# Kernel optimization log

Measured on AMD Instinct MI355X. Metric: run time of the kernel, lower is better.

Reference implementation:

```python
import jax, jax.numpy as jnp
import numpy as np

H, D = 8, 32  # gat_num_heads, structure_feature_dim // heads
N_CFG, E_CFG = 20000, 320000
N_DFG, E_DFG = 20000, 320000


def _gat(x, src, dst, lin, a_s, a_d, b):
    # PyG GATConv (concat=True), inference (dropout off). src/dst include self-loops.
    N = x.shape[0]
    xw = (x @ lin).reshape(N, H, D)              # [N,H,D]
    sc_s = (xw * a_s).sum(-1)                    # [N,H] att_src scores
    sc_d = (xw * a_d).sum(-1)                    # [N,H] att_dst scores
    alpha = jax.nn.leaky_relu(sc_s[src] + sc_d[dst], 0.2)   # [E,H]
    m = jax.lax.stop_gradient(jax.ops.segment_max(alpha, dst, num_segments=N))
    e = jnp.exp(alpha - m[dst])
    s = jax.ops.segment_sum(e, dst, num_segments=N)
    w = e / s[dst]                               # softmax over incoming edges per dst
    out = jax.ops.segment_sum(xw[src] * w[..., None], dst, num_segments=N)
    return out.reshape(N, H * D) + b


def _gat_stack(x, ei, params):
    N = x.shape[0]
    loops = jnp.arange(N)
    src = jnp.concatenate([ei[0], loops])        # add_self_loops=True (PyG default)
    dst = jnp.concatenate([ei[1], loops])
    for p in params:
        x = jax.nn.relu(_gat(x, src, dst, *p))
    return x.mean(0, keepdims=True)              # global_mean_pool -> [1, 256]


def _mha(x, in_w, in_b, out_w, out_b):
    # torch nn.MultiheadAttention, seq_len=1, batch=1, x:[1,256]
    qkv = x @ in_w.T + in_b                      # [1, 3*256]
    q, k, v = jnp.split(qkv, 3, axis=-1)
    q = q.reshape(1, H, D); k = k.reshape(1, H, D); v = v.reshape(1, H, D)
    scores = (q * k).sum(-1, keepdims=True) / jnp.sqrt(jnp.float32(D))
    attn = jax.nn.softmax(scores, axis=0)        # key length 1
    return (attn * v).reshape(1, H * D) @ out_w.T + out_b


def setup_inputs():
    key = jax.random.key(0)
    ks = iter(jax.random.split(key, 40))
    d = {}
    d['cfg_x'] = jax.random.normal(next(ks), (N_CFG, 64), jnp.float32)
    d['dfg_x'] = jax.random.normal(next(ks), (N_DFG, 32), jnp.float32)
    d['cfg_ei'] = jax.random.randint(next(ks), (2, E_CFG), 0, N_CFG)
    d['dfg_ei'] = jax.random.randint(next(ks), (2, E_DFG), 0, N_DFG)
    for name, in0 in (('cfg', 64), ('dfg', 32)):
        for i in range(3):
            fi = in0 if i == 0 else H * D
            s = 1.0 / np.sqrt(fi)
            d[f'{name}_lin{i}'] = jax.random.normal(next(ks), (fi, H * D), jnp.float32) * s
            d[f'{name}_as{i}'] = jax.random.normal(next(ks), (H, D), jnp.float32) * s
            d[f'{name}_ad{i}'] = jax.random.normal(next(ks), (H, D), jnp.float32) * s
            d[f'{name}_b{i}'] = jnp.zeros((H * D,), jnp.float32)
    E = H * D
    d['mha_in_w'] = jax.random.normal(next(ks), (3 * E, E), jnp.float32) / np.sqrt(E)
    d['mha_in_b'] = jnp.zeros((3 * E,), jnp.float32)
    d['mha_out_w'] = jax.random.normal(next(ks), (E, E), jnp.float32) / np.sqrt(E)
    d['mha_out_b'] = jnp.zeros((E,), jnp.float32)
    d['fus_w'] = jax.random.normal(next(ks), (E, 2 * E), jnp.float32) / np.sqrt(2 * E)
    d['fus_b'] = jnp.zeros((E,), jnp.float32)
    return d


def reference(cfg_x, dfg_x, cfg_ei, dfg_ei,
              cfg_lin0, cfg_as0, cfg_ad0, cfg_b0,
              cfg_lin1, cfg_as1, cfg_ad1, cfg_b1,
              cfg_lin2, cfg_as2, cfg_ad2, cfg_b2,
              dfg_lin0, dfg_as0, dfg_ad0, dfg_b0,
              dfg_lin1, dfg_as1, dfg_ad1, dfg_b1,
              dfg_lin2, dfg_as2, dfg_ad2, dfg_b2,
              mha_in_w, mha_in_b, mha_out_w, mha_out_b, fus_w, fus_b):
    cfg_p = [(cfg_lin0, cfg_as0, cfg_ad0, cfg_b0),
             (cfg_lin1, cfg_as1, cfg_ad1, cfg_b1),
             (cfg_lin2, cfg_as2, cfg_ad2, cfg_b2)]
    dfg_p = [(dfg_lin0, dfg_as0, dfg_ad0, dfg_b0),
             (dfg_lin1, dfg_as1, dfg_ad1, dfg_b1),
             (dfg_lin2, dfg_as2, dfg_ad2, dfg_b2)]
    cfg_f = _mha(_gat_stack(cfg_x, cfg_ei, cfg_p), mha_in_w, mha_in_b, mha_out_w, mha_out_b)
    dfg_f = _mha(_gat_stack(dfg_x, dfg_ei, dfg_p), mha_in_w, mha_in_b, mha_out_w, mha_out_b)
    return jnp.concatenate([cfg_f, dfg_f], axis=1) @ fus_w.T + fus_b
```

## Files before the change

### kernel.cpp

```cpp
#include <hip/hip_runtime.h>

#define NN 20000
#define ER 320000
#define ET 340000
#define CC 256
#define HH 8
#define DD 32


__global__ void zero_k(int* cnt, float* pooled) {
  int t = blockIdx.x * 256 + threadIdx.x;
  if (t < NN) cnt[t] = 0;
  if (pooled && t < 2 * CC) pooled[t] = 0.f;
}


__global__ void hist_k(const int* __restrict__ ei, int* __restrict__ cnt) {
  int e = blockIdx.x * 256 + threadIdx.x;
  if (e >= ET) return;
  int dst = (e < ER) ? ei[ER + e] : (e - ER);
  atomicAdd(&cnt[dst], 1);
}

__global__ __launch_bounds__(1024) void scan_k(const int* __restrict__ cnt,
                                               int* __restrict__ offs,
                                               int* __restrict__ cur) {
  __shared__ int part[1024];
  int t = threadIdx.x;
  const int CH = (NN + 1023) / 1024;
  int b = t * CH; if (b > NN) b = NN;
  int e = b + CH; if (e > NN) e = NN;
  int s = 0;
  for (int i = b; i < e; ++i) s += cnt[i];
  part[t] = s;
  __syncthreads();
  for (int off = 1; off < 1024; off <<= 1) {
    int v = (t >= off) ? part[t - off] : 0;
    __syncthreads();
    part[t] += v;
    __syncthreads();
  }
  int run = (t > 0) ? part[t - 1] : 0;
  for (int i = b; i < e; ++i) {
    int c = cnt[i];
    offs[i] = run;
    cur[i] = run;
    run += c;
  }
  if (t == 0) offs[NN] = ET;
}

__global__ void scatter_k(const int* __restrict__ ei, int* __restrict__ cur,
                          int* __restrict__ csr_src, int* __restrict__ csr_dst) {
  int e = blockIdx.x * 256 + threadIdx.x;
  if (e >= ET) return;
  int src, dst;
  if (e < ER) { src = ei[e]; dst = ei[ER + e]; }
  else        { src = dst = e - ER; }
  int pos = atomicAdd(&cur[dst], 1);
  csr_src[pos] = src;
  csr_dst[pos] = dst;
}

__global__ __launch_bounds__(256) void gemm_k(const float* __restrict__ X,
                                              const float* __restrict__ W,
                                              float* __restrict__ O, int K) {
  __shared__ float As[16][132];
  __shared__ float Bs[16][64];
  int tid = threadIdx.x;
  int tx = tid & 15;
  int ty = tid >> 4;
  int rb = blockIdx.y * 128, cb = blockIdx.x * 64;
  float acc[8][4] = {};

  for (int k0 = 0; k0 < K; k0 += 16) {
#pragma unroll
    for (int i = 0; i < 2; ++i) {
      int idx = tid + 256 * i;
      int row = idx >> 2;
      int kc = (idx & 3) * 4;
      int gr = rb + row; if (gr >= NN) gr = NN - 1;
      float4 v = *(const float4*)&X[(size_t)gr * K + k0 + kc];
      As[kc][row] = v.x; As[kc + 1][row] = v.y;
      As[kc + 2][row] = v.z; As[kc + 3][row] = v.w;
    }
    {
      int kk = tid >> 4, col = (tid & 15) * 4;
      float4 v = *(const float4*)&W[(size_t)(k0 + kk) * CC + cb + col];
      *(float4*)&Bs[kk][col] = v;
    }
    __syncthreads();
#pragma unroll
    for (int kk = 0; kk < 16; ++kk) {
      float4 a0 = *(const float4*)&As[kk][ty * 8];
      float4 a1 = *(const float4*)&As[kk][ty * 8 + 4];
      float4 b  = *(const float4*)&Bs[kk][tx * 4];
      float ar[8] = {a0.x, a0.y, a0.z, a0.w, a1.x, a1.y, a1.z, a1.w};
#pragma unroll
      for (int i = 0; i < 8; ++i) {
        acc[i][0] += ar[i] * b.x;
        acc[i][1] += ar[i] * b.y;
        acc[i][2] += ar[i] * b.z;
        acc[i][3] += ar[i] * b.w;
      }
    }
    __syncthreads();
  }
#pragma unroll
  for (int i = 0; i < 8; ++i) {
    int r = rb + ty * 8 + i;
    if (r < NN) {
      float4 v = make_float4(acc[i][0], acc[i][1], acc[i][2], acc[i][3]);
      *(float4*)&O[(size_t)r * CC + cb + tx * 4] = v;
    }
  }
}

__global__ void scores_k(const float* __restrict__ xw, const float* __restrict__ a_s,
                         const float* __restrict__ a_d, float* __restrict__ scs,
                         float* __restrict__ scd) {
  int t = blockIdx.x * blockDim.x + threadIdx.x;
  if (t >= NN * HH) return;
  int h = t & 7, n = t >> 3;
  const float* row = xw + (size_t)n * CC + h * DD;
  const float* as = a_s + h * DD;
  const float* ad = a_d + h * DD;
  float ss = 0.f, sd = 0.f;
#pragma unroll
  for (int d = 0; d < DD; ++d) {
    float v = row[d];
    ss += v * as[d];
    sd += v * ad[d];
  }
  scs[t] = ss;
  scd[t] = sd;
}

__global__ void alpha_k(const int* __restrict__ csr_src, const int* __restrict__ csr_dst,
                        const float* __restrict__ scs, const float* __restrict__ scd,
                        float* __restrict__ alpha) {
  int p = blockIdx.x * 256 + threadIdx.x;
  if (p >= ET) return;
  int s = csr_src[p], d = csr_dst[p];
  const float4* s4 = (const float4*)(scs + (size_t)s * 8);
  const float4* d4 = (const float4*)(scd + (size_t)d * 8);
  float4 a0 = s4[0], a1 = s4[1];
  float4 b0 = d4[0], b1 = d4[1];
  float4 r0, r1;
  float v;
  v = a0.x + b0.x; r0.x = v > 0.f ? v : 0.2f * v;
  v = a0.y + b0.y; r0.y = v > 0.f ? v : 0.2f * v;
  v = a0.z + b0.z; r0.z = v > 0.f ? v : 0.2f * v;
  v = a0.w + b0.w; r0.w = v > 0.f ? v : 0.2f * v;
  v = a1.x + b1.x; r1.x = v > 0.f ? v : 0.2f * v;
  v = a1.y + b1.y; r1.y = v > 0.f ? v : 0.2f * v;
  v = a1.z + b1.z; r1.z = v > 0.f ? v : 0.2f * v;
  v = a1.w + b1.w; r1.w = v > 0.f ? v : 0.2f * v;
  float4* o4 = (float4*)(alpha + (size_t)p * 8);
  o4[0] = r0; o4[1] = r1;
}

__global__ __launch_bounds__(256) void aggr_k(const float* __restrict__ xw,
                                              const float* __restrict__ alpha,
                                              const int* __restrict__ csr,
                                              const int* __restrict__ offs,
                                              const float* __restrict__ bias,
                                              float* __restrict__ out) {
  int n = blockIdx.x;
  int tid = threadIdx.x;
  int h = tid >> 5;
  int sl = tid & 31;
  int beg = offs[n], end = offs[n + 1];

  float m = -1e30f;
  for (int p = beg + sl; p < end; p += 32)
    m = fmaxf(m, alpha[(size_t)p * 8 + h]);
#pragma unroll
  for (int off = 16; off >= 1; off >>= 1)
    m = fmaxf(m, __shfl_xor(m, off, 64));

  float ssum = 0.f;
  for (int p = beg + sl; p < end; p += 32)
    ssum += __expf(alpha[(size_t)p * 8 + h] - m);
#pragma unroll
  for (int off = 16; off >= 1; off >>= 1)
    ssum += __shfl_xor(ssum, off, 64);
  float inv = 1.f / ssum;

  float acc = 0.f;
  int p = beg;
  for (; p + 2 <= end; p += 2) {
    int s0 = csr[p], s1 = csr[p + 1];
    float a0 = alpha[(size_t)p * 8 + h];
    float a1 = alpha[(size_t)(p + 1) * 8 + h];
    float x0 = xw[(size_t)s0 * CC + tid];
    float x1 = xw[(size_t)s1 * CC + tid];
    acc += x0 * (__expf(a0 - m) * inv);
    acc += x1 * (__expf(a1 - m) * inv);
  }
  if (p < end) {
    int s0 = csr[p];
    acc += xw[(size_t)s0 * CC + tid] * (__expf(alpha[(size_t)p * 8 + h] - m) * inv);
  }
  float r = acc + bias[tid];
  out[(size_t)n * CC + tid] = (r > 0.f) ? r : 0.f;
}

__global__ void pool_k(const float* __restrict__ x, float* __restrict__ pooled) {
  int tid = threadIdx.x;
  int rb = blockIdx.x * 250;
  float acc = 0.f;
  for (int r = 0; r < 250; ++r) acc += x[(size_t)(rb + r) * CC + tid];
  atomicAdd(&pooled[tid], acc * (1.f / NN));
}

__global__ __launch_bounds__(256) void head_k(const float* __restrict__ pooled,
                                              const float* __restrict__ in_w,
                                              const float* __restrict__ in_b,
                                              const float* __restrict__ out_w,
                                              const float* __restrict__ out_b,
                                              const float* __restrict__ fus_w,
                                              const float* __restrict__ fus_b,
                                              float* __restrict__ out) {
  __shared__ float v[2][CC];
  __shared__ float f[2][CC];
  int t = threadIdx.x;
  for (int g = 0; g < 2; ++g) {
    float a = in_b[2 * CC + t];
    const float* wr = &in_w[(size_t)(2 * CC + t) * CC];
    for (int k = 0; k < CC; ++k) a += pooled[g * CC + k] * wr[k];
    v[g][t] = a;
  }
  __syncthreads();
  for (int g = 0; g < 2; ++g) {
    float a = out_b[t];
    const float* wr = &out_w[(size_t)t * CC];
    for (int k = 0; k < CC; ++k) a += v[g][k] * wr[k];
    f[g][t] = a;
  }
  __syncthreads();
  float a = fus_b[t];
  const float* wr = &fus_w[(size_t)t * 2 * CC];
  const float* ff = &f[0][0];
  for (int k = 0; k < 2 * CC; ++k) a += ff[k] * wr[k];
  out[t] = a;
}

extern "C" void kernel_launch(void* const* d_in, const int* in_sizes, int n_in,
                              void* d_out, int out_size, void* d_ws, size_t ws_size,
                              hipStream_t stream) {
  const float* cfg_x = (const float*)d_in[0];
  const float* dfg_x = (const float*)d_in[1];
  const int* cfg_ei = (const int*)d_in[2];
  const int* dfg_ei = (const int*)d_in[3];
  const float *lin[2][3], *as_[2][3], *ad_[2][3], *bs_[2][3];
  for (int g = 0; g < 2; ++g)
    for (int i = 0; i < 3; ++i) {
      int base = 4 + g * 12 + i * 4;
      lin[g][i] = (const float*)d_in[base];
      as_[g][i] = (const float*)d_in[base + 1];
      ad_[g][i] = (const float*)d_in[base + 2];
      bs_[g][i] = (const float*)d_in[base + 3];
    }
  const float* mha_in_w = (const float*)d_in[28];
  const float* mha_in_b = (const float*)d_in[29];
  const float* mha_out_w = (const float*)d_in[30];
  const float* mha_out_b = (const float*)d_in[31];
  const float* fus_w = (const float*)d_in[32];
  const float* fus_b = (const float*)d_in[33];
  float* outp = (float*)d_out;

  char* w = (char*)d_ws;
  size_t o = 0;
  auto alloc = [&](size_t bytes) -> char* {
    char* p = w + o;
    o += (bytes + 255) & ~(size_t)255;
    return p;
  };
  float* bufA = (float*)alloc((size_t)NN * CC * 4);
  float* bufB = (float*)alloc((size_t)NN * CC * 4);
  float* scs = (float*)alloc((size_t)NN * HH * 4);
  float* scd = (float*)alloc((size_t)NN * HH * 4);
  float* alpha = (float*)alloc((size_t)ET * HH * 4);
  int* csr = (int*)alloc((size_t)ET * 4);
  int* csrd = (int*)alloc((size_t)ET * 4);
  int* offs = (int*)alloc((size_t)(NN + 1) * 4);
  int* cnt = (int*)alloc((size_t)NN * 4);
  int* cur = (int*)alloc((size_t)NN * 4);
  float* pooled = (float*)alloc(2 * CC * 4);

  const int* ei[2] = {cfg_ei, dfg_ei};
  const float* xin[2] = {cfg_x, dfg_x};
  const int K0[2] = {64, 32};

  for (int g = 0; g < 2; ++g) {
    zero_k<<<(NN + 255) / 256, 256, 0, stream>>>(cnt, g == 0 ? pooled : nullptr);
    hist_k<<<(ET + 255) / 256, 256, 0, stream>>>(ei[g], cnt);
    scan_k<<<1, 1024, 0, stream>>>(cnt, offs, cur);
    scatter_k<<<(ET + 255) / 256, 256, 0, stream>>>(ei[g], cur, csr, csrd);

    const float* x = xin[g];
    for (int l = 0; l < 3; ++l) {
      int K = (l == 0) ? K0[g] : CC;
      dim3 grid(CC / 64, (NN + 127) / 128);
      gemm_k<<<grid, 256, 0, stream>>>(x, lin[g][l], bufA, K);
      scores_k<<<(NN * HH + 255) / 256, 256, 0, stream>>>(bufA, as_[g][l], ad_[g][l],
                                                          scs, scd);
      alpha_k<<<(ET + 255) / 256, 256, 0, stream>>>(csr, csrd, scs, scd, alpha);
      aggr_k<<<NN, 256, 0, stream>>>(bufA, alpha, csr, offs, bs_[g][l], bufB);
      x = bufB;
    }
    pool_k<<<80, 256, 0, stream>>>(bufB, pooled + g * CC);
  }
  head_k<<<1, 256, 0, stream>>>(pooled, mha_in_w, mha_in_b, mha_out_w, mha_out_b,
                                fus_w, fus_b, outp);
}
```

Measured before the change: 1.025 ms.

## Split softmax into stats/weight kernels, unroll aggregation, retile GEMM, widen pooling

Segment-softmax statistics (max and inverse sum per destination and head) move out of the aggregation kernel into a dedicated wave-per-node kernel, and a separate pass rewrites alpha in place as normalized weights. The aggregation kernel then only does an 8-way unrolled gather-multiply-accumulate, so more independent loads are in flight per node. The GEMM now uses 128-thread blocks with an 8x8 register tile per thread, and pooling is spread over 400 blocks instead of 80. This costs two extra kernel launches and an extra read/write pass over alpha per layer, and the larger register tile may lower occupancy.

```diff
diff --git a/kernel.cpp b/kernel.cpp
--- a/kernel.cpp
+++ b/kernel.cpp
@@ -62,21 +62,21 @@
   csr_dst[pos] = dst;
 }
 
-__global__ __launch_bounds__(256) void gemm_k(const float* __restrict__ X,
+__global__ __launch_bounds__(128) void gemm_k(const float* __restrict__ X,
                                               const float* __restrict__ W,
                                               float* __restrict__ O, int K) {
   __shared__ float As[16][132];
-  __shared__ float Bs[16][64];
+  __shared__ float Bs[16][72];
   int tid = threadIdx.x;
-  int tx = tid & 15;
-  int ty = tid >> 4;
+  int tx = tid & 7;
+  int ty = tid >> 3;
   int rb = blockIdx.y * 128, cb = blockIdx.x * 64;
-  float acc[8][4] = {};
+  float acc[8][8] = {};
 
   for (int k0 = 0; k0 < K; k0 += 16) {
 #pragma unroll
-    for (int i = 0; i < 2; ++i) {
-      int idx = tid + 256 * i;
+    for (int i = 0; i < 4; ++i) {
+      int idx = tid + 128 * i;
       int row = idx >> 2;
       int kc = (idx & 3) * 4;
       int gr = rb + row; if (gr >= NN) gr = NN - 1;
@@ -84,25 +84,27 @@
       As[kc][row] = v.x; As[kc + 1][row] = v.y;
       As[kc + 2][row] = v.z; As[kc + 3][row] = v.w;
     }
-    {
-      int kk = tid >> 4, col = (tid & 15) * 4;
+#pragma unroll
+    for (int i = 0; i < 2; ++i) {
+      int idx = tid + 128 * i;
+      int kk = idx >> 4;
+      int col = (idx & 15) * 4;
       float4 v = *(const float4*)&W[(size_t)(k0 + kk) * CC + cb + col];
       *(float4*)&Bs[kk][col] = v;
     }
     __syncthreads();
 #pragma unroll
     for (int kk = 0; kk < 16; ++kk) {
-      float4 a0 = *(const float4*)&As[kk][ty * 8];
-      float4 a1 = *(const float4*)&As[kk][ty * 8 + 4];
-      float4 b  = *(const float4*)&Bs[kk][tx * 4];
-      float ar[8] = {a0.x, a0.y, a0.z, a0.w, a1.x, a1.y, a1.z, a1.w};
-#pragma unroll
-      for (int i = 0; i < 8; ++i) {
-        acc[i][0] += ar[i] * b.x;
-        acc[i][1] += ar[i] * b.y;
-        acc[i][2] += ar[i] * b.z;
-        acc[i][3] += ar[i] * b.w;
-      }
+      float a[8], b[8];
+      *(float4*)&a[0] = *(const float4*)&As[kk][ty * 8];
+      *(float4*)&a[4] = *(const float4*)&As[kk][ty * 8 + 4];
+      *(float4*)&b[0] = *(const float4*)&Bs[kk][tx * 8];
+      *(float4*)&b[4] = *(const float4*)&Bs[kk][tx * 8 + 4];
+#pragma unroll
+      for (int i = 0; i < 8; ++i)
+#pragma unroll
+        for (int j = 0; j < 8; ++j)
+          acc[i][j] += a[i] * b[j];
     }
     __syncthreads();
   }
@@ -110,8 +112,10 @@
   for (int i = 0; i < 8; ++i) {
     int r = rb + ty * 8 + i;
     if (r < NN) {
-      float4 v = make_float4(acc[i][0], acc[i][1], acc[i][2], acc[i][3]);
-      *(float4*)&O[(size_t)r * CC + cb + tx * 4] = v;
+      *(float4*)&O[(size_t)r * CC + cb + tx * 8] =
+          make_float4(acc[i][0], acc[i][1], acc[i][2], acc[i][3]);
+      *(float4*)&O[(size_t)r * CC + cb + tx * 8 + 4] =
+          make_float4(acc[i][4], acc[i][5], acc[i][6], acc[i][7]);
     }
   }
 }
@@ -160,8 +164,57 @@
   o4[0] = r0; o4[1] = r1;
 }
 
+__global__ __launch_bounds__(256) void stats_k(const float* __restrict__ alpha,
+                                               const int* __restrict__ offs,
+                                               float* __restrict__ ms,
+                                               float* __restrict__ inv) {
+  int wid = (blockIdx.x * 256 + threadIdx.x) >> 6;
+  if (wid >= NN) return;
+  int lane = threadIdx.x & 63;
+  int j = lane >> 3, h = lane & 7;
+  int beg = offs[wid], end = offs[wid + 1];
+  float m = -1e30f;
+  for (int p = beg + j; p < end; p += 8)
+    m = fmaxf(m, alpha[(size_t)p * 8 + h]);
+#pragma unroll
+  for (int off = 8; off <= 32; off <<= 1)
+    m = fmaxf(m, __shfl_xor(m, off, 64));
+  float s = 0.f;
+  for (int p = beg + j; p < end; p += 8)
+    s += __expf(alpha[(size_t)p * 8 + h] - m);
+#pragma unroll
+  for (int off = 8; off <= 32; off <<= 1)
+    s += __shfl_xor(s, off, 64);
+  if (lane < 8) {
+    ms[(size_t)wid * 8 + h] = m;
+    inv[(size_t)wid * 8 + h] = 1.f / s;
+  }
+}
+
+__global__ void wgt_k(float* __restrict__ alpha, const int* __restrict__ csr_dst,
+                      const float* __restrict__ ms, const float* __restrict__ inv) {
+  int p = blockIdx.x * 256 + threadIdx.x;
+  if (p >= ET) return;
+  int d = csr_dst[p];
+  float4* a4 = (float4*)(alpha + (size_t)p * 8);
+  const float4* m4 = (const float4*)(ms + (size_t)d * 8);
+  const float4* i4 = (const float4*)(inv + (size_t)d * 8);
+  float4 a0 = a4[0], a1 = a4[1];
+  float4 m0 = m4[0], m1 = m4[1];
+  float4 i0 = i4[0], i1 = i4[1];
+  a0.x = __expf(a0.x - m0.x) * i0.x;
+  a0.y = __expf(a0.y - m0.y) * i0.y;
+  a0.z = __expf(a0.z - m0.z) * i0.z;
+  a0.w = __expf(a0.w - m0.w) * i0.w;
+  a1.x = __expf(a1.x - m1.x) * i1.x;
+  a1.y = __expf(a1.y - m1.y) * i1.y;
+  a1.z = __expf(a1.z - m1.z) * i1.z;
+  a1.w = __expf(a1.w - m1.w) * i1.w;
+  a4[0] = a0; a4[1] = a1;
+}
+
 __global__ __launch_bounds__(256) void aggr_k(const float* __restrict__ xw,
-                                              const float* __restrict__ alpha,
+                                              const float* __restrict__ w,
                                               const int* __restrict__ csr,
                                               const int* __restrict__ offs,
                                               const float* __restrict__ bias,
@@ -169,48 +222,42 @@
   int n = blockIdx.x;
   int tid = threadIdx.x;
   int h = tid >> 5;
-  int sl = tid & 31;
   int beg = offs[n], end = offs[n + 1];
-
-  float m = -1e30f;
-  for (int p = beg + sl; p < end; p += 32)
-    m = fmaxf(m, alpha[(size_t)p * 8 + h]);
-#pragma unroll
-  for (int off = 16; off >= 1; off >>= 1)
-    m = fmaxf(m, __shfl_xor(m, off, 64));
-
-  float ssum = 0.f;
-  for (int p = beg + sl; p < end; p += 32)
-    ssum += __expf(alpha[(size_t)p * 8 + h] - m);
-#pragma unroll
-  for (int off = 16; off >= 1; off >>= 1)
-    ssum += __shfl_xor(ssum, off, 64);
-  float inv = 1.f / ssum;
-
   float acc = 0.f;
   int p = beg;
-  for (; p + 2 <= end; p += 2) {
-    int s0 = csr[p], s1 = csr[p + 1];
-    float a0 = alpha[(size_t)p * 8 + h];
-    float a1 = alpha[(size_t)(p + 1) * 8 + h];
-    float x0 = xw[(size_t)s0 * CC + tid];
-    float x1 = xw[(size_t)s1 * CC + tid];
-    acc += x0 * (__expf(a0 - m) * inv);
-    acc += x1 * (__expf(a1 - m) * inv);
-  }
-  if (p < end) {
-    int s0 = csr[p];
-    acc += xw[(size_t)s0 * CC + tid] * (__expf(alpha[(size_t)p * 8 + h] - m) * inv);
-  }
+  for (; p + 8 <= end; p += 8) {
+    int s[8]; float wv[8]; float x[8];
+#pragma unroll
+    for (int i = 0; i < 8; ++i) s[i] = csr[p + i];
+#pragma unroll
+    for (int i = 0; i < 8; ++i) wv[i] = w[(size_t)(p + i) * 8 + h];
+#pragma unroll
+    for (int i = 0; i < 8; ++i) x[i] = xw[(size_t)s[i] * CC + tid];
+#pragma unroll
+    for (int i = 0; i < 8; ++i) acc += wv[i] * x[i];
+  }
+  for (; p + 4 <= end; p += 4) {
+    int s[4]; float wv[4]; float x[4];
+#pragma unroll
+    for (int i = 0; i < 4; ++i) s[i] = csr[p + i];
+#pragma unroll
+    for (int i = 0; i < 4; ++i) wv[i] = w[(size_t)(p + i) * 8 + h];
+#pragma unroll
+    for (int i = 0; i < 4; ++i) x[i] = xw[(size_t)s[i] * CC + tid];
+#pragma unroll
+    for (int i = 0; i < 4; ++i) acc += wv[i] * x[i];
+  }
+  for (; p < end; ++p)
+    acc += w[(size_t)p * 8 + h] * xw[(size_t)csr[p] * CC + tid];
   float r = acc + bias[tid];
   out[(size_t)n * CC + tid] = (r > 0.f) ? r : 0.f;
 }
 
 __global__ void pool_k(const float* __restrict__ x, float* __restrict__ pooled) {
   int tid = threadIdx.x;
-  int rb = blockIdx.x * 250;
+  int rb = blockIdx.x * 50;
   float acc = 0.f;
-  for (int r = 0; r < 250; ++r) acc += x[(size_t)(rb + r) * CC + tid];
+  for (int r = 0; r < 50; ++r) acc += x[(size_t)(rb + r) * CC + tid];
   atomicAdd(&pooled[tid], acc * (1.f / NN));
 }
 
@@ -281,6 +328,8 @@
   float* bufB = (float*)alloc((size_t)NN * CC * 4);
   float* scs = (float*)alloc((size_t)NN * HH * 4);
   float* scd = (float*)alloc((size_t)NN * HH * 4);
+  float* ms = (float*)alloc((size_t)NN * HH * 4);
+  float* inv = (float*)alloc((size_t)NN * HH * 4);
   float* alpha = (float*)alloc((size_t)ET * HH * 4);
   int* csr = (int*)alloc((size_t)ET * 4);
   int* csrd = (int*)alloc((size_t)ET * 4);
@@ -303,14 +352,16 @@
     for (int l = 0; l < 3; ++l) {
       int K = (l == 0) ? K0[g] : CC;
       dim3 grid(CC / 64, (NN + 127) / 128);
-      gemm_k<<<grid, 256, 0, stream>>>(x, lin[g][l], bufA, K);
+      gemm_k<<<grid, 128, 0, stream>>>(x, lin[g][l], bufA, K);
       scores_k<<<(NN * HH + 255) / 256, 256, 0, stream>>>(bufA, as_[g][l], ad_[g][l],
                                                           scs, scd);
       alpha_k<<<(ET + 255) / 256, 256, 0, stream>>>(csr, csrd, scs, scd, alpha);
+      stats_k<<<(NN * 64 + 255) / 256, 256, 0, stream>>>(alpha, offs, ms, inv);
+      wgt_k<<<(ET + 255) / 256, 256, 0, stream>>>(alpha, csrd, ms, inv);
       aggr_k<<<NN, 256, 0, stream>>>(bufA, alpha, csr, offs, bs_[g][l], bufB);
       x = bufB;
     }
-    pool_k<<<80, 256, 0, stream>>>(bufB, pooled + g * CC);
+    pool_k<<<(NN / 50), 256, 0, stream>>>(bufB, pooled + g * CC);
   }
   head_k<<<1, 256, 0, stream>>>(pooled, mha_in_w, mha_in_b, mha_out_w, mha_out_b,
                                 fus_w, fus_b, outp);
```

Result: slower. 1.098 ms (+7.1%).
